# Optimization experiments

Measured on AMD Instinct MI355X. Metric: run time of the kernel, lower is better.

The kernel has to match this reference:

```python
import jax, jax.numpy as jnp
import numpy as np

EMPTY, TRUE, FALSE = 0.0, 1.0, 2.0  # MemoryVal ternary encoding

B = 2048          # batch
IN_BITS = 4096    # raw input bits
N_IN, N_ST, N_OUT = 2048, 1024, 1024
K = 14            # bits (connections) per neuron -> memory_size = 2**K
M = 2 ** K


def setup_inputs() -> dict:
    key = jax.random.key(0)
    ks = jax.random.split(key, 8)
    return {
        "input_bits": jax.random.randint(ks[0], (B, IN_BITS), 0, 2, dtype=jnp.int32),
        "state_bits": jax.random.randint(ks[1], (B, N_ST), 0, 2, dtype=jnp.int32),
        "in_conn": jax.random.randint(ks[2], (N_IN, K), 0, IN_BITS, dtype=jnp.int32),
        "in_mem": jax.random.randint(ks[3], (N_IN, M), 0, 3).astype(jnp.float32),
        "st_conn": jax.random.randint(ks[4], (N_ST, K), 0, N_IN + N_ST, dtype=jnp.int32),
        "st_mem": jax.random.randint(ks[5], (N_ST, M), 0, 3).astype(jnp.float32),
        "out_conn": jax.random.randint(ks[6], (N_OUT, K), 0, N_IN + N_ST, dtype=jnp.int32),
        "out_mem": jax.random.randint(ks[7], (N_OUT, M), 0, 3).astype(jnp.float32),
    }


def _ram_layer(bits, conn, mem):
    """bits: [B, T] 0/1; conn: [N, K] indices into T; mem: [N, 2**K] ternary."""
    k = conn.shape[1]
    g = bits[:, conn].astype(jnp.int32)                      # [B, N, K] gathered local bits
    w = (2 ** jnp.arange(k - 1, -1, -1)).astype(jnp.int32)   # MSB-first packing (matches _get_desired_bits)
    addr = jnp.sum(g * w, axis=-1)                           # [B, N] memory addresses
    vals = mem[jnp.arange(mem.shape[0])[None, :], addr]      # [B, N] per-neuron LUT lookup
    return jnp.where(vals == TRUE, 1.0, 0.0).astype(jnp.float32)  # neuron fires iff TRUE


def reference(input_bits, state_bits, in_conn, in_mem, st_conn, st_mem, out_conn, out_mem):
    h_in = _ram_layer(input_bits, in_conn, in_mem)                          # [B, N_IN]
    s_inp = jnp.concatenate([h_in, state_bits.astype(h_in.dtype)], axis=1)  # [B, N_IN+N_ST]
    s_out = _ram_layer(s_inp, st_conn, st_mem)                              # [B, N_ST]
    o_inp = jnp.concatenate([h_in, s_out], axis=1)                          # [B, N_IN+N_ST]
    return _ram_layer(o_inp, out_conn, out_mem)                             # [B, N_OUT]
```

## Files before the change

kernel.cpp:

```cpp
#include <hip/hip_runtime.h>
#include <stdint.h>

#define BATCH   2048
#define IN_BITS 4096
#define N_IN    2048
#define N_ST    1024
#define N_OUT   1024
#define KBITS   14
#define MW      512
#define SROW    96

#define IM4 8388608
#define SM4 4194304
#define OM4 4194304
#define GS  524288

typedef float f32x4 __attribute__((ext_vector_type(4)));
typedef int   i32x4 __attribute__((ext_vector_type(4)));

__global__ __launch_bounds__(256) void pack_mem_all(const float* __restrict__ im,
                                                    const float* __restrict__ sm,
                                                    const float* __restrict__ om,
                                                    uint32_t* __restrict__ im_p,
                                                    uint32_t* __restrict__ sm_p,
                                                    uint32_t* __restrict__ om_p) {
    const int t = blockIdx.x * 256 + threadIdx.x;
    const int lane = threadIdx.x & 63;
#pragma unroll
    for (int c = 0; c < 32; ++c) {
        const float* s; uint32_t* d; int cl;
        if (c < 16)      { s = im; d = im_p; cl = c; }
        else if (c < 24) { s = sm; d = sm_p; cl = c - 16; }
        else             { s = om; d = om_p; cl = c - 24; }
        const long i = (long)cl * GS + t;
        f32x4 v = __builtin_nontemporal_load((const f32x4*)s + i);
        unsigned long long b0 = __ballot(v[0] == 1.0f);
        unsigned long long b1 = __ballot(v[1] == 1.0f);
        unsigned long long b2 = __ballot(v[2] == 1.0f);
        unsigned long long b3 = __ballot(v[3] == 1.0f);
        if (lane < 8) {
            unsigned long long bj = (lane & 4) ? ((lane & 2) ? b3 : b2)
                                               : ((lane & 2) ? b1 : b0);
            uint32_t w = (lane & 1) ? (uint32_t)(bj >> 32) : (uint32_t)bj;
            d[((i >> 6) << 3) + lane] = w;
        }
    }
}

__global__ __launch_bounds__(256) void pack_input(const int* __restrict__ src,
                                                  uint32_t* __restrict__ dst) {
    const int t = blockIdx.x * 256 + threadIdx.x;
    const int lane = threadIdx.x & 63;
#pragma unroll
    for (int c = 0; c < 4; ++c) {
        const long i = (long)c * GS + t;
        i32x4 v = __builtin_nontemporal_load((const i32x4*)src + i);
        unsigned long long b0 = __ballot(v[0] == 1);
        unsigned long long b1 = __ballot(v[1] == 1);
        unsigned long long b2 = __ballot(v[2] == 1);
        unsigned long long b3 = __ballot(v[3] == 1);
        if (lane < 8) {
            unsigned long long bj = (lane & 4) ? ((lane & 2) ? b3 : b2)
                                               : ((lane & 2) ? b1 : b0);
            uint32_t w = (lane & 1) ? (uint32_t)(bj >> 32) : (uint32_t)bj;
            dst[((i >> 6) << 3) + lane] = w;
        }
    }
}

__global__ __launch_bounds__(256) void pack_state(const int4* __restrict__ src,
                                                  uint32_t* __restrict__ dst) {
    int t = blockIdx.x * 256 + threadIdx.x;
    int4 v = src[t];
    uint32_t nib = (uint32_t)(v.x == 1) | ((uint32_t)(v.y == 1) << 1) |
                   ((uint32_t)(v.z == 1) << 2) | ((uint32_t)(v.w == 1) << 3);
    int lane = threadIdx.x & 63;
    uint32_t w = nib << (4 * (lane & 7));
    w |= __shfl_xor(w, 1, 64);
    w |= __shfl_xor(w, 2, 64);
    w |= __shfl_xor(w, 4, 64);
    if ((lane & 7) == 0) {
        int g = t >> 3;
        int r = g >> 5;
        int c = g & 31;
        dst[(long)r * SROW + 64 + c] = w;
    }
}

template <int SRCW, int BCHUNK, int MODE>
__global__ __launch_bounds__(256) void ram_layer(const uint32_t* __restrict__ src,
                                                 const int* __restrict__ conn,
                                                 const uint32_t* __restrict__ memp,
                                                 uint32_t* __restrict__ dst0,
                                                 uint32_t* __restrict__ dst1,
                                                 float* __restrict__ fout) {
    __shared__ uint32_t lds[BCHUNK * SRCW];
    const int tid = threadIdx.x;
    const int b0 = blockIdx.y * BCHUNK;

    {
        const uint4* g = (const uint4*)(src + (long)b0 * SRCW);
        uint4* l = (uint4*)lds;
        constexpr int NV = BCHUNK * SRCW / 4;
        for (int i = tid; i < NV; i += 256) l[i] = g[i];
    }
    __syncthreads();

    const int n = blockIdx.x * 256 + tid;
    int wd[KBITS], sh[KBITS];
#pragma unroll
    for (int k = 0; k < KBITS; k++) {
        int idx = conn[n * KBITS + k];
        if (SRCW == 128) {
            wd[k] = ((idx >> 5) & ~7) | ((idx & 3) << 1) | ((idx >> 7) & 1);
            sh[k] = (idx >> 2) & 31;
        } else {
            wd[k] = idx >> 5;
            sh[k] = idx & 31;
        }
    }
    const uint32_t* mrow = memp + (long)n * MW;
    const int lane = tid & 63;
    const int nbase = blockIdx.x * 256 + (tid & ~63);

#pragma unroll 4
    for (int bb = 0; bb < BCHUNK; ++bb) {
        const uint32_t* row = lds + bb * SRCW;
        uint32_t addr = 0;
#pragma unroll
        for (int k = 0; k < KBITS; k++)
            addr = (addr << 1) | ((row[wd[k]] >> sh[k]) & 1u);
        uint32_t mw = ((addr >> 5) & ~7u) | ((addr & 3u) << 1) | ((addr >> 7) & 1u);
        uint32_t bit = (mrow[mw] >> ((addr >> 2) & 31u)) & 1u;
        const int b = b0 + bb;
        if (MODE == 2) {
            fout[(long)b * N_OUT + n] = (float)bit;
        } else {
            unsigned long long m = __ballot(bit != 0);
            if (lane == 0) {
                if (MODE == 0) {
                    *(unsigned long long*)(dst0 + (long)b * SROW + (nbase >> 5)) = m;
                    *(unsigned long long*)(dst1 + (long)b * SROW + (nbase >> 5)) = m;
                } else {
                    *(unsigned long long*)(dst0 + (long)b * SROW + 64 + (nbase >> 5)) = m;
                }
            }
        }
    }
}

extern "C" void kernel_launch(void* const* d_in, const int* in_sizes, int n_in,
                              void* d_out, int out_size, void* d_ws, size_t ws_size,
                              hipStream_t stream) {
    const int*   input_bits = (const int*)d_in[0];
    const int*   state_bits = (const int*)d_in[1];
    const int*   in_conn    = (const int*)d_in[2];
    const float* in_mem     = (const float*)d_in[3];
    const int*   st_conn    = (const int*)d_in[4];
    const float* st_mem     = (const float*)d_in[5];
    const int*   out_conn   = (const int*)d_in[6];
    const float* out_mem    = (const float*)d_in[7];
    float*       out        = (float*)d_out;

    char* ws = (char*)d_ws;
    uint32_t* bits1 = (uint32_t*)(ws);
    uint32_t* buf_s = (uint32_t*)(ws + 1048576);
    uint32_t* buf_o = (uint32_t*)(ws + 1048576 + 786432);
    uint32_t* im_p  = (uint32_t*)(ws + 1048576 + 2 * 786432);
    uint32_t* sm_p  = (uint32_t*)(ws + 1048576 + 2 * 786432 + 4194304);
    uint32_t* om_p  = (uint32_t*)(ws + 1048576 + 2 * 786432 + 4194304 + 2097152);

    pack_input<<<2048, 256, 0, stream>>>(input_bits, bits1);
    pack_state<<<(BATCH * N_ST / 4) / 256, 256, 0, stream>>>((const int4*)state_bits, buf_s);
    pack_mem_all<<<2048, 256, 0, stream>>>(in_mem, st_mem, out_mem, im_p, sm_p, om_p);

    ram_layer<128, 16, 0><<<dim3(N_IN / 256, BATCH / 16), 256, 0, stream>>>(
        bits1, in_conn, im_p, buf_s, buf_o, nullptr);
    ram_layer<SROW, 8, 1><<<dim3(N_ST / 256, BATCH / 8), 256, 0, stream>>>(
        buf_s, st_conn, sm_p, buf_o, nullptr, nullptr);
    ram_layer<SROW, 8, 2><<<dim3(N_OUT / 256, BATCH / 8), 256, 0, stream>>>(
        buf_o, out_conn, om_p, nullptr, nullptr, out);
}
```

Measured before the change: 336.5 us.

## Transpose RAM layer mapping: lanes over batch, waves loop over neurons

The RAM layer kernel now assigns one batch row per lane and has each wave iterate over 16 neurons. Connection indices become wave-uniform scalar loads, and the LDS rows are padded by one word so that per-lane row reads avoid bank conflicts. Output bits are accumulated per lane and written as 16-bit stores instead of ballots. In exchange, the packed-memory lookups become scattered per lane across batches rather than per neuron row, the final layer writes floats with a large stride between lanes, and each 64-batch tile is loaded into LDS more times overall.

```diff
diff --git a/kernel.cpp b/kernel.cpp
--- a/kernel.cpp
+++ b/kernel.cpp
@@ -87,65 +87,71 @@
     }
 }
 
-template <int SRCW, int BCHUNK, int MODE>
-__global__ __launch_bounds__(256) void ram_layer(const uint32_t* __restrict__ src,
-                                                 const int* __restrict__ conn,
-                                                 const uint32_t* __restrict__ memp,
-                                                 uint32_t* __restrict__ dst0,
-                                                 uint32_t* __restrict__ dst1,
-                                                 float* __restrict__ fout) {
-    __shared__ uint32_t lds[BCHUNK * SRCW];
+template <int SRCW, int MODE>
+__global__ __launch_bounds__(256) void ram_layer_t(const uint32_t* __restrict__ src,
+                                                   const int* __restrict__ conn,
+                                                   const uint32_t* __restrict__ memp,
+                                                   uint32_t* __restrict__ dst0,
+                                                   uint32_t* __restrict__ dst1,
+                                                   float* __restrict__ fout) {
+    constexpr int LSTR = SRCW + 1;
+    __shared__ uint32_t lds[64 * LSTR];
     const int tid = threadIdx.x;
-    const int b0 = blockIdx.y * BCHUNK;
+    const int b0 = blockIdx.y * 64;
 
     {
         const uint4* g = (const uint4*)(src + (long)b0 * SRCW);
-        uint4* l = (uint4*)lds;
-        constexpr int NV = BCHUNK * SRCW / 4;
-        for (int i = tid; i < NV; i += 256) l[i] = g[i];
+        constexpr int NQ = 64 * SRCW / 4;
+#pragma unroll
+        for (int i = tid; i < NQ; i += 256) {
+            uint4 v = g[i];
+            int r = i / (SRCW / 4);
+            int w = (i - r * (SRCW / 4)) * 4;
+            uint32_t* p = &lds[r * LSTR + w];
+            p[0] = v.x; p[1] = v.y; p[2] = v.z; p[3] = v.w;
+        }
     }
     __syncthreads();
 
-    const int n = blockIdx.x * 256 + tid;
-    int wd[KBITS], sh[KBITS];
+    const int lane = tid & 63;
+    const int wave = __builtin_amdgcn_readfirstlane(tid >> 6);
+    const int nw0 = blockIdx.x * 64 + wave * 16;
+    const long b = b0 + lane;
+    const uint32_t* row = lds + lane * LSTR;
+
+    uint32_t acc = 0;
+#pragma unroll 2
+    for (int j = 0; j < 16; ++j) {
+        const int n = nw0 + j;
+        const int* cp = conn + n * KBITS;
+        uint32_t addr = 0;
 #pragma unroll
-    for (int k = 0; k < KBITS; k++) {
-        int idx = conn[n * KBITS + k];
-        if (SRCW == 128) {
-            wd[k] = ((idx >> 5) & ~7) | ((idx & 3) << 1) | ((idx >> 7) & 1);
-            sh[k] = (idx >> 2) & 31;
+        for (int k = 0; k < KBITS; ++k) {
+            int idx = cp[k];
+            int wd, sh;
+            if (SRCW == 128) {
+                wd = ((idx >> 5) & ~7) | ((idx & 3) << 1) | ((idx >> 7) & 1);
+                sh = (idx >> 2) & 31;
+            } else {
+                wd = idx >> 5;
+                sh = idx & 31;
+            }
+            addr = (addr << 1) | ((row[wd] >> sh) & 1u);
+        }
+        uint32_t mw = ((addr >> 5) & ~7u) | ((addr & 3u) << 1) | ((addr >> 7) & 1u);
+        uint32_t bit = (memp[(long)n * MW + mw] >> ((addr >> 2) & 31u)) & 1u;
+        if (MODE == 2) {
+            fout[b * N_OUT + n] = (float)bit;
         } else {
-            wd[k] = idx >> 5;
-            sh[k] = idx & 31;
+            acc |= bit << j;
         }
     }
-    const uint32_t* mrow = memp + (long)n * MW;
-    const int lane = tid & 63;
-    const int nbase = blockIdx.x * 256 + (tid & ~63);
-
-#pragma unroll 4
-    for (int bb = 0; bb < BCHUNK; ++bb) {
-        const uint32_t* row = lds + bb * SRCW;
-        uint32_t addr = 0;
-#pragma unroll
-        for (int k = 0; k < KBITS; k++)
-            addr = (addr << 1) | ((row[wd[k]] >> sh[k]) & 1u);
-        uint32_t mw = ((addr >> 5) & ~7u) | ((addr & 3u) << 1) | ((addr >> 7) & 1u);
-        uint32_t bit = (mrow[mw] >> ((addr >> 2) & 31u)) & 1u;
-        const int b = b0 + bb;
-        if (MODE == 2) {
-            fout[(long)b * N_OUT + n] = (float)bit;
-        } else {
-            unsigned long long m = __ballot(bit != 0);
-            if (lane == 0) {
-                if (MODE == 0) {
-                    *(unsigned long long*)(dst0 + (long)b * SROW + (nbase >> 5)) = m;
-                    *(unsigned long long*)(dst1 + (long)b * SROW + (nbase >> 5)) = m;
-                } else {
-                    *(unsigned long long*)(dst0 + (long)b * SROW + 64 + (nbase >> 5)) = m;
-                }
-            }
-        }
+    if (MODE != 2) {
+        const int woff = (MODE == 0 ? 0 : 64) + (nw0 >> 5);
+        const int half = (nw0 >> 4) & 1;
+        ((ushort*)(dst0 + b * SROW + woff))[half] = (ushort)acc;
+        if (MODE == 0)
+            ((ushort*)(dst1 + b * SROW + woff))[half] = (ushort)acc;
     }
 }
 
@@ -174,10 +180,10 @@
     pack_state<<<(BATCH * N_ST / 4) / 256, 256, 0, stream>>>((const int4*)state_bits, buf_s);
     pack_mem_all<<<2048, 256, 0, stream>>>(in_mem, st_mem, out_mem, im_p, sm_p, om_p);
 
-    ram_layer<128, 16, 0><<<dim3(N_IN / 256, BATCH / 16), 256, 0, stream>>>(
+    ram_layer_t<128, 0><<<dim3(N_IN / 64, BATCH / 64), 256, 0, stream>>>(
         bits1, in_conn, im_p, buf_s, buf_o, nullptr);
-    ram_layer<SROW, 8, 1><<<dim3(N_ST / 256, BATCH / 8), 256, 0, stream>>>(
+    ram_layer_t<SROW, 1><<<dim3(N_ST / 64, BATCH / 64), 256, 0, stream>>>(
         buf_s, st_conn, sm_p, buf_o, nullptr, nullptr);
-    ram_layer<SROW, 8, 2><<<dim3(N_OUT / 256, BATCH / 8), 256, 0, stream>>>(
+    ram_layer_t<SROW, 2><<<dim3(N_OUT / 64, BATCH / 64), 256, 0, stream>>>(
         buf_o, out_conn, om_p, nullptr, nullptr, out);
 }
```

New measurement: 339.3 us. Within noise of the previous version (+0.8%).
